# Performance work log

Hardware: AMD Instinct MI355X
Metric: run time of the kernel (lower is better)

## Reference

```python
import jax, jax.numpy as jnp
import numpy as np

B, T, F, E = 256, 256, 8, 128
H = 2 * E  # hidden_dim = 2*embedding_dim = 256
NL = 5     # num_layers per LSTM stack


def setup_inputs() -> dict:
    key = jax.random.key(0)
    ks = jax.random.split(key, 9)
    s1 = 1.0 / np.sqrt(H)
    s2 = 1.0 / np.sqrt(E)
    u = lambda k, shape, s: jax.random.uniform(k, shape, jnp.float32, -s, s)
    return {
        "x": jax.random.normal(ks[0], (B, T, F), jnp.float32),
        # stack 1: input F -> hidden H, 5 layers. b = b_ih + b_hh combined.
        "w_ih0_1": u(ks[1], (4 * H, F), s1),
        "w_ihr_1": u(ks[2], (NL - 1, 4 * H, H), s1),
        "w_hh_1": u(ks[3], (NL, 4 * H, H), s1),
        "b_1": u(ks[4], (NL, 4 * H), s1),
        # stack 2: input H -> hidden E, 5 layers
        "w_ih0_2": u(ks[5], (4 * E, H), s2),
        "w_ihr_2": u(ks[6], (NL - 1, 4 * E, E), s2),
        "w_hh_2": u(ks[7], (NL, 4 * E, E), s2),
        "b_2": u(ks[8], (NL, 4 * E), s2),
    }


def _lstm_layer(x, w_ih, w_hh, b):
    """x: [B,T,D] -> (outputs [B,T,Hd], final hidden [B,Hd]). PyTorch gate order i,f,g,o."""
    Hd = w_hh.shape[-1]
    # precompute input contribution for all timesteps (the big GEMM)
    xg = jnp.einsum('btd,gd->tbg', x, w_ih) + b  # [T,B,4Hd]
    h0 = jnp.zeros((x.shape[0], Hd), x.dtype)

    def step(carry, xt):
        h, c = carry
        g = xt + h @ w_hh.T
        i, f, gg, o = jnp.split(g, 4, axis=-1)
        c = jax.nn.sigmoid(f) * c + jax.nn.sigmoid(i) * jnp.tanh(gg)
        h = jax.nn.sigmoid(o) * jnp.tanh(c)
        return (h, c), h

    (h, _), hs = jax.lax.scan(step, (h0, h0), xg)
    return jnp.swapaxes(hs, 0, 1), h


def _stack(x, w_ih0, w_ihr, w_hh, b):
    y, h = _lstm_layer(x, w_ih0, w_hh[0], b[0])
    for l in range(1, w_hh.shape[0]):
        y, h = _lstm_layer(y, w_ihr[l - 1], w_hh[l], b[l])
    return y, h


def reference(x, w_ih0_1, w_ihr_1, w_hh_1, b_1, w_ih0_2, w_ihr_2, w_hh_2, b_2):
    x = x.reshape(x.shape[0], T, F)
    y, _ = _stack(x, w_ih0_1, w_ihr_1, w_hh_1, b_1)   # [B,T,H]
    _, h = _stack(y, w_ih0_2, w_ihr_2, w_hh_2, b_2)   # h: [B,E] last layer final hidden
    return h
```

## Files before the change

kernel.cpp:

```cpp
#include <hip/hip_runtime.h>
#include <math.h>

typedef unsigned short u16;
typedef unsigned int   u32;
typedef unsigned long long u64;
typedef __bf16 bf16x8 __attribute__((ext_vector_type(8)));
typedef float  f32x4  __attribute__((ext_vector_type(4)));

#define BB 256
#define TT 256
#define HD 256
#define ED 128
#define DEPTH 8
#define NE 73

#define HRING   (10 * DEPTH * BB * HD / 2)
#define CTR_OFF (2 * HRING)
#define GRP_OFF (CTR_OFF + 512)
#define XP_U32  (BB * TT * 8 / 2)
#define XPH_OFF (GRP_OFF + 640)
#define XPL_OFF (XPH_OFF + XP_U32)
#define WT_OFF  (XPL_OFF + XP_U32)

__constant__ size_t g_woff[10] = {0ul,589824ul,1638400ul,2686976ul,3735552ul,
                                  4784128ul,5177344ul,5439488ul,5701632ul,5963776ul};
__constant__ int g_cb[11] = {0,73728,204800,335872,466944,598016,
                             647168,679936,712704,745472,778240};

__device__ __forceinline__ u16 f2bf_hi(float f) {
    u32 u = __float_as_uint(f);
    u32 r = (u + 0x7FFFu + ((u >> 16) & 1u)) >> 16;
    return (u16)r;
}
__device__ __forceinline__ float bf2f(u16 h) { return __uint_as_float(((u32)h) << 16); }
__device__ __forceinline__ float sigmoidf_(float v) { return 1.0f / (1.0f + expf(-v)); }

__global__ __launch_bounds__(256) void zero_state(u32* wsd) {
    const int n = XPH_OFF;
    for (int i = blockIdx.x * blockDim.x + threadIdx.x; i < n; i += gridDim.x * blockDim.x)
        wsd[i] = 0u;
}

__global__ __launch_bounds__(256) void conv_x(const float* __restrict__ x, u32* __restrict__ wsd) {
    u16* xph = (u16*)(wsd + XPH_OFF);
    u16* xpl = (u16*)(wsd + XPL_OFF);
    const int n = BB * TT * 8;
    for (int i = blockIdx.x * blockDim.x + threadIdx.x; i < n; i += gridDim.x * blockDim.x) {
        float v = x[i];
        u16 hi = f2bf_hi(v);
        xph[i] = hi;
        xpl[i] = f2bf_hi(v - bf2f(hi));
    }
}

__global__ __launch_bounds__(256) void conv_all(
    const float* __restrict__ w_ih0_1, const float* __restrict__ w_ihr_1,
    const float* __restrict__ w_hh_1,
    const float* __restrict__ w_ih0_2, const float* __restrict__ w_ihr_2,
    const float* __restrict__ w_hh_2,
    u32* __restrict__ wsd)
{
    __bf16* dst0 = (__bf16*)(wsd + WT_OFF);
    const int nch = 778240;
    for (int ci = blockIdx.x * blockDim.x + threadIdx.x; ci < nch;
         ci += gridDim.x * blockDim.x) {
        int l = 0;
        while (ci >= g_cb[l + 1]) ++l;
        int di = ci - g_cb[l];

        const int hd  = (l < 5) ? 256 : 128;
        const int din = (l == 0) ? 32 : ((l < 6) ? 256 : 128);
        const int xw  = (l == 0) ? 8 : din;
        const int Kp  = din + hd;
        const int nk  = Kp >> 5;

        const float *wih, *whh; int wihld, whhld;
        if (l == 0)      { wih = w_ih0_1;                                whh = w_hh_1;
                           wihld = 8;   whhld = 256; }
        else if (l < 5)  { wih = w_ihr_1 + (size_t)(l - 1) * 1024 * 256; whh = w_hh_1 + (size_t)l * 1024 * 256;
                           wihld = 256; whhld = 256; }
        else if (l == 5) { wih = w_ih0_2;                                whh = w_hh_2;
                           wihld = 256; whhld = 128; }
        else             { wih = w_ihr_2 + (size_t)(l - 6) * 512 * 128;  whh = w_hh_2 + (size_t)(l - 5) * 512 * 128;
                           wihld = 128; whhld = 128; }

        int lane = di & 63;
        int rem  = di >> 6;
        int kt   = rem % nk;
        int rem2 = rem / nk;
        int p    = rem2 & 1;
        int g    = (rem2 >> 1) & 3;
        int jt   = rem2 >> 3;
        int r15  = lane & 15, kq = lane >> 4;
        int row  = g * hd + jt * 16 + r15;

        bf16x8 o8;
        #pragma unroll
        for (int e = 0; e < 8; ++e) {
            int k = kt * 32 + kq * 8 + e;
            float v = 0.0f;
            if (k < xw) v = wih[(size_t)row * wihld + k];
            else if (k >= din && k < Kp) v = whh[(size_t)row * whhld + (k - din)];
            __bf16 h = (__bf16)v;
            o8[e] = p ? (__bf16)(v - (float)h) : h;
        }
        *(bf16x8*)(dst0 + g_woff[l] + (size_t)di * 8) = o8;
    }
}

template<int NKI, int NKT, bool ISL0>
__device__ void run_persist(int l, int bid, int xcd, int jt, int bt, int hd, u32 arr7,
    int ng, u32* __restrict__ gflg,
    const float* __restrict__ bias, u32* __restrict__ wsd, u32* __restrict__ ctr,
    float* __restrict__ out, const u16* __restrict__ A_sh)
{
    constexpr int DIN = NKI * 32;
    constexpr int RS  = (NKT < 4) ? NKT : 4;

    u16* hhi = (u16*)wsd;
    u16* hlo = (u16*)(wsd + HRING);
    const u16* xph = (const u16*)(wsd + XPH_OFF);
    const u16* xpl = (const u16*)(wsd + XPL_OFF);

    const int tid  = threadIdx.x;
    const int lane = tid & 63;
    const int wv   = tid >> 6;
    const int r15  = lane & 15;
    const int kqc  = lane >> 4;
    const int brow = bt * 128 + wv * 16 + r15;
    const int j0   = jt * 16 + kqc * 4;

    float bgr[4][4];
    #pragma unroll
    for (int g = 0; g < 4; ++g) {
        float4 v = *(const float4*)&bias[g * hd + j0];
        bgr[g][0] = v.x; bgr[g][1] = v.y; bgr[g][2] = v.z; bgr[g][3] = v.w;
    }

    int offH[4], offL[4];
    #pragma unroll
    for (int g = 0; g < 4; ++g) {
        offH[g] = (g * 2)     * NKT * 512 + lane * 8;
        offL[g] = (g * 2 + 1) * NKT * 512 + lane * 8;
    }

    float4 cv = make_float4(0.f, 0.f, 0.f, 0.f);
    const int lm = (l > 0) ? (l - 1) : 0;

    auto STEP = [&](int t) {
        const size_t sIn   = ((size_t)lm * DEPTH + (t & 7)) * (BB * HD);
        const size_t sPrev = ((size_t)l * DEPTH + ((t - 1) & 7)) * (BB * HD);
        const size_t sOut  = ((size_t)l * DEPTH + (t & 7)) * (BB * HD);

        auto ldB = [&](int kt, uint4& H4, uint4& L4) {
            if constexpr (ISL0) {
                if (kt == 0) {
                    if (kqc == 0) {
                        const size_t xo = ((size_t)brow * TT + t) * 8;
                        H4 = *(const uint4*)(xph + xo);
                        L4 = *(const uint4*)(xpl + xo);
                    } else { H4 = make_uint4(0,0,0,0); L4 = make_uint4(0,0,0,0); }
                } else {
                    const size_t o = sPrev + (size_t)brow * HD + (kt * 32 - 32) + kqc * 8;
                    H4 = *(const uint4*)(hhi + o);
                    L4 = *(const uint4*)(hlo + o);
                }
            } else {
                const int k0 = kt * 32 + kqc * 8;
                const size_t o = (k0 < DIN) ? (sIn + (size_t)brow * HD + k0)
                                            : (sPrev + (size_t)brow * HD + (k0 - DIN));
                H4 = *(const uint4*)(hhi + o);
                L4 = *(const uint4*)(hlo + o);
            }
        };

        f32x4 acc0 = {0.f,0.f,0.f,0.f}, acc1 = {0.f,0.f,0.f,0.f};
        f32x4 acc2 = {0.f,0.f,0.f,0.f}, acc3 = {0.f,0.f,0.f,0.f};

        uint4 ra[RS], rb[RS];
        #pragma unroll
        for (int i = 0; i < RS; ++i) ldB(i, ra[i], rb[i]);

        #pragma unroll
        for (int kt = 0; kt < NKT; ++kt) {
            union { uint4 u; bf16x8 v; } BH, BL;
            BH.u = ra[kt % RS]; BL.u = rb[kt % RS];
            bf16x8 bh = BH.v, bl = BL.v;
            if (kt + RS < NKT) ldB(kt + RS, ra[kt % RS], rb[kt % RS]);

            const int kof = kt * 512;
            bf16x8 a0h = *(const bf16x8*)&A_sh[offH[0] + kof];
            bf16x8 a1h = *(const bf16x8*)&A_sh[offH[1] + kof];
            bf16x8 a2h = *(const bf16x8*)&A_sh[offH[2] + kof];
            bf16x8 a3h = *(const bf16x8*)&A_sh[offH[3] + kof];
            bf16x8 a0l = *(const bf16x8*)&A_sh[offL[0] + kof];
            bf16x8 a1l = *(const bf16x8*)&A_sh[offL[1] + kof];
            bf16x8 a2l = *(const bf16x8*)&A_sh[offL[2] + kof];
            bf16x8 a3l = *(const bf16x8*)&A_sh[offL[3] + kof];

            acc0 = __builtin_amdgcn_mfma_f32_16x16x32_bf16(a0h, bh, acc0, 0, 0, 0);
            acc1 = __builtin_amdgcn_mfma_f32_16x16x32_bf16(a1h, bh, acc1, 0, 0, 0);
            acc2 = __builtin_amdgcn_mfma_f32_16x16x32_bf16(a2h, bh, acc2, 0, 0, 0);
            acc3 = __builtin_amdgcn_mfma_f32_16x16x32_bf16(a3h, bh, acc3, 0, 0, 0);
            acc0 = __builtin_amdgcn_mfma_f32_16x16x32_bf16(a0h, bl, acc0, 0, 0, 0);
            acc1 = __builtin_amdgcn_mfma_f32_16x16x32_bf16(a1h, bl, acc1, 0, 0, 0);
            acc2 = __builtin_amdgcn_mfma_f32_16x16x32_bf16(a2h, bl, acc2, 0, 0, 0);
            acc3 = __builtin_amdgcn_mfma_f32_16x16x32_bf16(a3h, bl, acc3, 0, 0, 0);
            acc0 = __builtin_amdgcn_mfma_f32_16x16x32_bf16(a0l, bh, acc0, 0, 0, 0);
            acc1 = __builtin_amdgcn_mfma_f32_16x16x32_bf16(a1l, bh, acc1, 0, 0, 0);
            acc2 = __builtin_amdgcn_mfma_f32_16x16x32_bf16(a2l, bh, acc2, 0, 0, 0);
            acc3 = __builtin_amdgcn_mfma_f32_16x16x32_bf16(a3l, bh, acc3, 0, 0, 0);
        }

        float4 hv;
        {
            float i_, f_, g_, o_;
            i_ = sigmoidf_(acc0[0] + bgr[0][0]); f_ = sigmoidf_(acc1[0] + bgr[1][0]);
            g_ = tanhf   (acc2[0] + bgr[2][0]); o_ = sigmoidf_(acc3[0] + bgr[3][0]);
            cv.x = fmaf(f_, cv.x, i_ * g_); hv.x = o_ * tanhf(cv.x);
            i_ = sigmoidf_(acc0[1] + bgr[0][1]); f_ = sigmoidf_(acc1[1] + bgr[1][1]);
            g_ = tanhf   (acc2[1] + bgr[2][1]); o_ = sigmoidf_(acc3[1] + bgr[3][1]);
            cv.y = fmaf(f_, cv.y, i_ * g_); hv.y = o_ * tanhf(cv.y);
            i_ = sigmoidf_(acc0[2] + bgr[0][2]); f_ = sigmoidf_(acc1[2] + bgr[1][2]);
            g_ = tanhf   (acc2[2] + bgr[2][2]); o_ = sigmoidf_(acc3[2] + bgr[3][2]);
            cv.z = fmaf(f_, cv.z, i_ * g_); hv.z = o_ * tanhf(cv.z);
            i_ = sigmoidf_(acc0[3] + bgr[0][3]); f_ = sigmoidf_(acc1[3] + bgr[1][3]);
            g_ = tanhf   (acc2[3] + bgr[2][3]); o_ = sigmoidf_(acc3[3] + bgr[3][3]);
            cv.w = fmaf(f_, cv.w, i_ * g_); hv.w = o_ * tanhf(cv.w);
        }

        u16 h0 = f2bf_hi(hv.x), h1 = f2bf_hi(hv.y), h2 = f2bf_hi(hv.z), h3 = f2bf_hi(hv.w);
        u64 hiP = (u64)h0 | ((u64)h1 << 16) | ((u64)h2 << 32) | ((u64)h3 << 48);
        u64 loP = (u64)f2bf_hi(hv.x - bf2f(h0)) |
                  ((u64)f2bf_hi(hv.y - bf2f(h1)) << 16) |
                  ((u64)f2bf_hi(hv.z - bf2f(h2)) << 32) |
                  ((u64)f2bf_hi(hv.w - bf2f(h3)) << 48);
        const size_t ho = sOut + (size_t)brow * HD + j0;
        __hip_atomic_store((u64*)(hhi + ho), hiP, __ATOMIC_RELAXED, __HIP_MEMORY_SCOPE_AGENT);
        __hip_atomic_store((u64*)(hlo + ho), loP, __ATOMIC_RELAXED, __HIP_MEMORY_SCOPE_AGENT);

        if (l == 9 && t == TT - 1)
            *(float4*)&out[(size_t)brow * ED + j0] = hv;
    };

    for (int E = 0; E < NE; ++E) {
        const int ep = E - l;
        if (ep >= 0 && ep < 64) {
            #pragma unroll 1
            for (int i = 0; i < 4; ++i) {
                const int t = 4 * ep + i;
                if (i > 0) {
                    if (tid == 0) {
                        const u32 tg = (u32)ng * (u32)(3 * ep + i);
                        for (int it = 0; it < (1 << 20); ++it) {
                            if (__hip_atomic_load(gflg, __ATOMIC_RELAXED,
                                                  __HIP_MEMORY_SCOPE_AGENT) >= tg) break;
                            __builtin_amdgcn_s_sleep(1);
                        }
                    }
                    __syncthreads();
                }
                STEP(t);
                if (i < 3) {
                    __syncthreads();
                    if (tid == 0)
                        __hip_atomic_fetch_add(gflg, 1u, __ATOMIC_RELAXED, __HIP_MEMORY_SCOPE_AGENT);
                }
            }
        }

        __syncthreads();
        if (tid == 0) {
            __hip_atomic_fetch_add(&ctr[xcd * 32], 1u,
                                   __ATOMIC_RELAXED, __HIP_MEMORY_SCOPE_AGENT);
            const u32 w1 = (u32)(E + 1);
            if (bid == 0) {
                for (int it = 0; it < (1 << 22); ++it) {
                    bool ok = true;
                    #pragma unroll
                    for (int r = 0; r < 8; ++r) {
                        u32 tgt = ((r == 7) ? arr7 : 32u) * w1;
                        ok &= (__hip_atomic_load(&ctr[r * 32], __ATOMIC_RELAXED,
                                                 __HIP_MEMORY_SCOPE_AGENT) >= tgt);
                    }
                    if (ok) break;
                    __builtin_amdgcn_s_sleep(1);
                }
                __hip_atomic_store(&ctr[256], w1, __ATOMIC_RELAXED, __HIP_MEMORY_SCOPE_AGENT);
            } else {
                for (int it = 0; it < (1 << 22); ++it) {
                    if (__hip_atomic_load(&ctr[256], __ATOMIC_RELAXED,
                                          __HIP_MEMORY_SCOPE_AGENT) >= w1) break;
                    __builtin_amdgcn_s_sleep(1);
                }
            }
            __builtin_amdgcn_fence(__ATOMIC_ACQUIRE, "agent");
        }
        __syncthreads();
    }
}

__global__ __launch_bounds__(512, 2) void lstm_persist(
    const float* __restrict__ b_1, const float* __restrict__ b_2,
    u32* __restrict__ wsd, float* __restrict__ out)
{
    __shared__ __align__(16) u16 A_sh[65536];

    const int bid = blockIdx.x;
    const int xcd = bid & 7, slot = bid >> 3;
    int l, jt, bt;
    if (xcd < 5)      { l = xcd;               bt = slot >> 4;        jt = slot & 15; }
    else if (xcd == 5){ l = 5 + (slot >> 4);   bt = (slot >> 3) & 1;  jt = slot & 7; }
    else if (xcd == 6){ l = 7 + (slot >> 4);   bt = (slot >> 3) & 1;  jt = slot & 7; }
    else              { if (slot >= 16) return; l = 9; bt = slot >> 3; jt = slot & 7; }

    const int hd  = (l < 5) ? 256 : 128;
    const int din = (l == 0) ? 32 : ((l < 6) ? 256 : 128);
    const int nk  = (din + hd) >> 5;
    const float* bias = (l < 5) ? (b_1 + l * 1024) : (b_2 + (l - 5) * 512);

    u32* ctr  = wsd + CTR_OFF;
    u32* gflg = wsd + GRP_OFF + (size_t)(l * 2 + bt) * 32;
    const u16* wt = (const u16*)(wsd + WT_OFF);

    const int ng = (l < 5) ? 16 : 8;

    {
        const uint4* src = (const uint4*)(wt + g_woff[l] + (size_t)jt * 8 * nk * 512);
        uint4* dst = (uint4*)A_sh;
        const int n4 = nk * 512;
        for (int i = threadIdx.x; i < n4; i += 512) dst[i] = src[i];
    }
    __syncthreads();

    if (l == 0)
        run_persist<1, 9, true >(l, bid, xcd, jt, bt, hd, 16u, ng, gflg, bias, wsd, ctr, out, A_sh);
    else if (l < 5)
        run_persist<8, 16, false>(l, bid, xcd, jt, bt, hd, 16u, ng, gflg, bias, wsd, ctr, out, A_sh);
    else if (l == 5)
        run_persist<8, 12, false>(l, bid, xcd, jt, bt, hd, 16u, ng, gflg, bias, wsd, ctr, out, A_sh);
    else
        run_persist<4, 8, false>(l, bid, xcd, jt, bt, hd, 16u, ng, gflg, bias, wsd, ctr, out, A_sh);
}

extern "C" void kernel_launch(void* const* d_in, const int* in_sizes, int n_in,
                              void* d_out, int out_size, void* d_ws, size_t ws_size,
                              hipStream_t stream) {
    const float* x       = (const float*)d_in[0];
    const float* w_ih0_1 = (const float*)d_in[1];
    const float* w_ihr_1 = (const float*)d_in[2];
    const float* w_hh_1  = (const float*)d_in[3];
    const float* b_1     = (const float*)d_in[4];
    const float* w_ih0_2 = (const float*)d_in[5];
    const float* w_ihr_2 = (const float*)d_in[6];
    const float* w_hh_2  = (const float*)d_in[7];
    const float* b_2     = (const float*)d_in[8];
    u32*   wsd = (u32*)d_ws;
    float* out = (float*)d_out;

    hipLaunchKernelGGL(zero_state, dim3(1024), dim3(256), 0, stream, wsd);
    hipLaunchKernelGGL(conv_all, dim3(1024), dim3(256), 0, stream,
                       w_ih0_1, w_ihr_1, w_hh_1, w_ih0_2, w_ihr_2, w_hh_2, wsd);
    hipLaunchKernelGGL(conv_x, dim3(256), dim3(256), 0, stream, x, wsd);
    hipLaunchKernelGGL(lstm_persist, dim3(256), dim3(512), 0, stream,
                       b_1, b_2, wsd, out);
}
```

Before: 2.890 ms.

## Hoist input-projection MFMAs off the recurrent critical path, pairing two timesteps

Splits each LSTM step into an input-projection part and a recurrent part. The input contribution for two consecutive timesteps is computed together before the inter-block wait, so each weight fragment loaded from LDS feeds two B operands. Only the recurrent h·W_hh part stays between the grid-flag waits, which shortens the serialized per-step chain. The cost is a second set of accumulators, which raises register pressure and may lower occupancy or cause spills.

```diff
diff --git a/kernel.cpp b/kernel.cpp
--- a/kernel.cpp
+++ b/kernel.cpp
@@ -34,6 +34,9 @@
 }
 __device__ __forceinline__ float bf2f(u16 h) { return __uint_as_float(((u32)h) << 16); }
 __device__ __forceinline__ float sigmoidf_(float v) { return 1.0f / (1.0f + expf(-v)); }
+__device__ __forceinline__ bf16x8 asbf8(const uint4& u) {
+    union { uint4 u; bf16x8 v; } c; c.u = u; return c.v;
+}
 
 __global__ __launch_bounds__(256) void zero_state(u32* wsd) {
     const int n = XPH_OFF;
@@ -114,8 +117,9 @@
     const float* __restrict__ bias, u32* __restrict__ wsd, u32* __restrict__ ctr,
     float* __restrict__ out, const u16* __restrict__ A_sh)
 {
-    constexpr int DIN = NKI * 32;
-    constexpr int RS  = (NKT < 4) ? NKT : 4;
+    constexpr int NKR = NKT - NKI;
+    constexpr int RS  = (NKR < 4) ? NKR : 4;
+    constexpr int RSI = (NKI < 3) ? NKI : 3;
 
     u16* hhi = (u16*)wsd;
     u16* hlo = (u16*)(wsd + HRING);
@@ -147,85 +151,136 @@
     float4 cv = make_float4(0.f, 0.f, 0.f, 0.f);
     const int lm = (l > 0) ? (l - 1) : 0;
 
-    auto STEP = [&](int t) {
-        const size_t sIn   = ((size_t)lm * DEPTH + (t & 7)) * (BB * HD);
+    auto MF12 = [&](int kof, const bf16x8& bh, const bf16x8& bl, f32x4 (&ac)[4]) {
+        bf16x8 a0h = *(const bf16x8*)&A_sh[offH[0] + kof];
+        bf16x8 a1h = *(const bf16x8*)&A_sh[offH[1] + kof];
+        bf16x8 a2h = *(const bf16x8*)&A_sh[offH[2] + kof];
+        bf16x8 a3h = *(const bf16x8*)&A_sh[offH[3] + kof];
+        bf16x8 a0l = *(const bf16x8*)&A_sh[offL[0] + kof];
+        bf16x8 a1l = *(const bf16x8*)&A_sh[offL[1] + kof];
+        bf16x8 a2l = *(const bf16x8*)&A_sh[offL[2] + kof];
+        bf16x8 a3l = *(const bf16x8*)&A_sh[offL[3] + kof];
+        ac[0] = __builtin_amdgcn_mfma_f32_16x16x32_bf16(a0h, bh, ac[0], 0, 0, 0);
+        ac[1] = __builtin_amdgcn_mfma_f32_16x16x32_bf16(a1h, bh, ac[1], 0, 0, 0);
+        ac[2] = __builtin_amdgcn_mfma_f32_16x16x32_bf16(a2h, bh, ac[2], 0, 0, 0);
+        ac[3] = __builtin_amdgcn_mfma_f32_16x16x32_bf16(a3h, bh, ac[3], 0, 0, 0);
+        ac[0] = __builtin_amdgcn_mfma_f32_16x16x32_bf16(a0h, bl, ac[0], 0, 0, 0);
+        ac[1] = __builtin_amdgcn_mfma_f32_16x16x32_bf16(a1h, bl, ac[1], 0, 0, 0);
+        ac[2] = __builtin_amdgcn_mfma_f32_16x16x32_bf16(a2h, bl, ac[2], 0, 0, 0);
+        ac[3] = __builtin_amdgcn_mfma_f32_16x16x32_bf16(a3h, bl, ac[3], 0, 0, 0);
+        ac[0] = __builtin_amdgcn_mfma_f32_16x16x32_bf16(a0l, bh, ac[0], 0, 0, 0);
+        ac[1] = __builtin_amdgcn_mfma_f32_16x16x32_bf16(a1l, bh, ac[1], 0, 0, 0);
+        ac[2] = __builtin_amdgcn_mfma_f32_16x16x32_bf16(a2l, bh, ac[2], 0, 0, 0);
+        ac[3] = __builtin_amdgcn_mfma_f32_16x16x32_bf16(a3l, bh, ac[3], 0, 0, 0);
+    };
+    auto MF24 = [&](int kof, const bf16x8& b0h, const bf16x8& b0l,
+                    const bf16x8& b1h, const bf16x8& b1l,
+                    f32x4 (&a0)[4], f32x4 (&a1)[4]) {
+        bf16x8 a0h = *(const bf16x8*)&A_sh[offH[0] + kof];
+        bf16x8 a1hh = *(const bf16x8*)&A_sh[offH[1] + kof];
+        bf16x8 a2h = *(const bf16x8*)&A_sh[offH[2] + kof];
+        bf16x8 a3h = *(const bf16x8*)&A_sh[offH[3] + kof];
+        bf16x8 a0l = *(const bf16x8*)&A_sh[offL[0] + kof];
+        bf16x8 a1l = *(const bf16x8*)&A_sh[offL[1] + kof];
+        bf16x8 a2l = *(const bf16x8*)&A_sh[offL[2] + kof];
+        bf16x8 a3l = *(const bf16x8*)&A_sh[offL[3] + kof];
+        a0[0] = __builtin_amdgcn_mfma_f32_16x16x32_bf16(a0h,  b0h, a0[0], 0, 0, 0);
+        a1[0] = __builtin_amdgcn_mfma_f32_16x16x32_bf16(a0h,  b1h, a1[0], 0, 0, 0);
+        a0[1] = __builtin_amdgcn_mfma_f32_16x16x32_bf16(a1hh, b0h, a0[1], 0, 0, 0);
+        a1[1] = __builtin_amdgcn_mfma_f32_16x16x32_bf16(a1hh, b1h, a1[1], 0, 0, 0);
+        a0[2] = __builtin_amdgcn_mfma_f32_16x16x32_bf16(a2h,  b0h, a0[2], 0, 0, 0);
+        a1[2] = __builtin_amdgcn_mfma_f32_16x16x32_bf16(a2h,  b1h, a1[2], 0, 0, 0);
+        a0[3] = __builtin_amdgcn_mfma_f32_16x16x32_bf16(a3h,  b0h, a0[3], 0, 0, 0);
+        a1[3] = __builtin_amdgcn_mfma_f32_16x16x32_bf16(a3h,  b1h, a1[3], 0, 0, 0);
+        a0[0] = __builtin_amdgcn_mfma_f32_16x16x32_bf16(a0h,  b0l, a0[0], 0, 0, 0);
+        a1[0] = __builtin_amdgcn_mfma_f32_16x16x32_bf16(a0h,  b1l, a1[0], 0, 0, 0);
+        a0[1] = __builtin_amdgcn_mfma_f32_16x16x32_bf16(a1hh, b0l, a0[1], 0, 0, 0);
+        a1[1] = __builtin_amdgcn_mfma_f32_16x16x32_bf16(a1hh, b1l, a1[1], 0, 0, 0);
+        a0[2] = __builtin_amdgcn_mfma_f32_16x16x32_bf16(a2h,  b0l, a0[2], 0, 0, 0);
+        a1[2] = __builtin_amdgcn_mfma_f32_16x16x32_bf16(a2h,  b1l, a1[2], 0, 0, 0);
+        a0[3] = __builtin_amdgcn_mfma_f32_16x16x32_bf16(a3h,  b0l, a0[3], 0, 0, 0);
+        a1[3] = __builtin_amdgcn_mfma_f32_16x16x32_bf16(a3h,  b1l, a1[3], 0, 0, 0);
+        a0[0] = __builtin_amdgcn_mfma_f32_16x16x32_bf16(a0l,  b0h, a0[0], 0, 0, 0);
+        a1[0] = __builtin_amdgcn_mfma_f32_16x16x32_bf16(a0l,  b1h, a1[0], 0, 0, 0);
+        a0[1] = __builtin_amdgcn_mfma_f32_16x16x32_bf16(a1l,  b0h, a0[1], 0, 0, 0);
+        a1[1] = __builtin_amdgcn_mfma_f32_16x16x32_bf16(a1l,  b1h, a1[1], 0, 0, 0);
+        a0[2] = __builtin_amdgcn_mfma_f32_16x16x32_bf16(a2l,  b0h, a0[2], 0, 0, 0);
+        a1[2] = __builtin_amdgcn_mfma_f32_16x16x32_bf16(a2l,  b1h, a1[2], 0, 0, 0);
+        a0[3] = __builtin_amdgcn_mfma_f32_16x16x32_bf16(a3l,  b0h, a0[3], 0, 0, 0);
+        a1[3] = __builtin_amdgcn_mfma_f32_16x16x32_bf16(a3l,  b1h, a1[3], 0, 0, 0);
+    };
+
+    auto DUAL_IN = [&](int t0, f32x4 (&a0)[4], f32x4 (&a1)[4]) {
+        if constexpr (ISL0) {
+            uint4 h0, l0q, h1, l1q;
+            if (kqc == 0) {
+                const size_t x0 = ((size_t)brow * TT + t0) * 8;
+                const size_t x1 = ((size_t)brow * TT + t0 + 1) * 8;
+                h0 = *(const uint4*)(xph + x0); l0q = *(const uint4*)(xpl + x0);
+                h1 = *(const uint4*)(xph + x1); l1q = *(const uint4*)(xpl + x1);
+            } else {
+                h0 = make_uint4(0,0,0,0); l0q = h0; h1 = h0; l1q = h0;
+            }
+            MF24(0, asbf8(h0), asbf8(l0q), asbf8(h1), asbf8(l1q), a0, a1);
+        } else {
+            const size_t sIn0 = ((size_t)lm * DEPTH + (t0 & 7)) * (BB * HD);
+            const size_t sIn1 = ((size_t)lm * DEPTH + ((t0 + 1) & 7)) * (BB * HD);
+            auto ldBI = [&](size_t sIn, int kt, uint4& H4, uint4& L4) {
+                const size_t o = sIn + (size_t)brow * HD + kt * 32 + kqc * 8;
+                H4 = *(const uint4*)(hhi + o);
+                L4 = *(const uint4*)(hlo + o);
+            };
+            uint4 p0a[RSI], p0b[RSI], p1a[RSI], p1b[RSI];
+            #pragma unroll
+            for (int i = 0; i < RSI; ++i) {
+                ldBI(sIn0, i, p0a[i], p0b[i]);
+                ldBI(sIn1, i, p1a[i], p1b[i]);
+            }
+            #pragma unroll
+            for (int kt = 0; kt < NKI; ++kt) {
+                bf16x8 b0h = asbf8(p0a[kt % RSI]), b0l = asbf8(p0b[kt % RSI]);
+                bf16x8 b1h = asbf8(p1a[kt % RSI]), b1l = asbf8(p1b[kt % RSI]);
+                if (kt + RSI < NKI) {
+                    ldBI(sIn0, kt + RSI, p0a[kt % RSI], p0b[kt % RSI]);
+                    ldBI(sIn1, kt + RSI, p1a[kt % RSI], p1b[kt % RSI]);
+                }
+                MF24(kt * 512, b0h, b0l, b1h, b1l, a0, a1);
+            }
+        }
+    };
+
+    auto REC_STEP = [&](int t, f32x4 (&ac)[4]) {
         const size_t sPrev = ((size_t)l * DEPTH + ((t - 1) & 7)) * (BB * HD);
         const size_t sOut  = ((size_t)l * DEPTH + (t & 7)) * (BB * HD);
-
-        auto ldB = [&](int kt, uint4& H4, uint4& L4) {
-            if constexpr (ISL0) {
-                if (kt == 0) {
-                    if (kqc == 0) {
-                        const size_t xo = ((size_t)brow * TT + t) * 8;
-                        H4 = *(const uint4*)(xph + xo);
-                        L4 = *(const uint4*)(xpl + xo);
-                    } else { H4 = make_uint4(0,0,0,0); L4 = make_uint4(0,0,0,0); }
-                } else {
-                    const size_t o = sPrev + (size_t)brow * HD + (kt * 32 - 32) + kqc * 8;
-                    H4 = *(const uint4*)(hhi + o);
-                    L4 = *(const uint4*)(hlo + o);
-                }
-            } else {
-                const int k0 = kt * 32 + kqc * 8;
-                const size_t o = (k0 < DIN) ? (sIn + (size_t)brow * HD + k0)
-                                            : (sPrev + (size_t)brow * HD + (k0 - DIN));
-                H4 = *(const uint4*)(hhi + o);
-                L4 = *(const uint4*)(hlo + o);
-            }
+        auto ldBR = [&](int kt, uint4& H4, uint4& L4) {
+            const size_t o = sPrev + (size_t)brow * HD + (kt - NKI) * 32 + kqc * 8;
+            H4 = *(const uint4*)(hhi + o);
+            L4 = *(const uint4*)(hlo + o);
         };
-
-        f32x4 acc0 = {0.f,0.f,0.f,0.f}, acc1 = {0.f,0.f,0.f,0.f};
-        f32x4 acc2 = {0.f,0.f,0.f,0.f}, acc3 = {0.f,0.f,0.f,0.f};
-
         uint4 ra[RS], rb[RS];
         #pragma unroll
-        for (int i = 0; i < RS; ++i) ldB(i, ra[i], rb[i]);
-
+        for (int i = 0; i < RS; ++i) ldBR(NKI + i, ra[i], rb[i]);
         #pragma unroll
-        for (int kt = 0; kt < NKT; ++kt) {
-            union { uint4 u; bf16x8 v; } BH, BL;
-            BH.u = ra[kt % RS]; BL.u = rb[kt % RS];
-            bf16x8 bh = BH.v, bl = BL.v;
-            if (kt + RS < NKT) ldB(kt + RS, ra[kt % RS], rb[kt % RS]);
-
-            const int kof = kt * 512;
-            bf16x8 a0h = *(const bf16x8*)&A_sh[offH[0] + kof];
-            bf16x8 a1h = *(const bf16x8*)&A_sh[offH[1] + kof];
-            bf16x8 a2h = *(const bf16x8*)&A_sh[offH[2] + kof];
-            bf16x8 a3h = *(const bf16x8*)&A_sh[offH[3] + kof];
-            bf16x8 a0l = *(const bf16x8*)&A_sh[offL[0] + kof];
-            bf16x8 a1l = *(const bf16x8*)&A_sh[offL[1] + kof];
-            bf16x8 a2l = *(const bf16x8*)&A_sh[offL[2] + kof];
-            bf16x8 a3l = *(const bf16x8*)&A_sh[offL[3] + kof];
-
-            acc0 = __builtin_amdgcn_mfma_f32_16x16x32_bf16(a0h, bh, acc0, 0, 0, 0);
-            acc1 = __builtin_amdgcn_mfma_f32_16x16x32_bf16(a1h, bh, acc1, 0, 0, 0);
-            acc2 = __builtin_amdgcn_mfma_f32_16x16x32_bf16(a2h, bh, acc2, 0, 0, 0);
-            acc3 = __builtin_amdgcn_mfma_f32_16x16x32_bf16(a3h, bh, acc3, 0, 0, 0);
-            acc0 = __builtin_amdgcn_mfma_f32_16x16x32_bf16(a0h, bl, acc0, 0, 0, 0);
-            acc1 = __builtin_amdgcn_mfma_f32_16x16x32_bf16(a1h, bl, acc1, 0, 0, 0);
-            acc2 = __builtin_amdgcn_mfma_f32_16x16x32_bf16(a2h, bl, acc2, 0, 0, 0);
-            acc3 = __builtin_amdgcn_mfma_f32_16x16x32_bf16(a3h, bl, acc3, 0, 0, 0);
-            acc0 = __builtin_amdgcn_mfma_f32_16x16x32_bf16(a0l, bh, acc0, 0, 0, 0);
-            acc1 = __builtin_amdgcn_mfma_f32_16x16x32_bf16(a1l, bh, acc1, 0, 0, 0);
-            acc2 = __builtin_amdgcn_mfma_f32_16x16x32_bf16(a2l, bh, acc2, 0, 0, 0);
-            acc3 = __builtin_amdgcn_mfma_f32_16x16x32_bf16(a3l, bh, acc3, 0, 0, 0);
+        for (int kt = NKI; kt < NKT; ++kt) {
+            bf16x8 bh = asbf8(ra[(kt - NKI) % RS]), bl = asbf8(rb[(kt - NKI) % RS]);
+            if (kt + RS < NKT) ldBR(kt + RS, ra[(kt - NKI) % RS], rb[(kt - NKI) % RS]);
+            MF12(kt * 512, bh, bl, ac);
         }
 
         float4 hv;
         {
             float i_, f_, g_, o_;
-            i_ = sigmoidf_(acc0[0] + bgr[0][0]); f_ = sigmoidf_(acc1[0] + bgr[1][0]);
-            g_ = tanhf   (acc2[0] + bgr[2][0]); o_ = sigmoidf_(acc3[0] + bgr[3][0]);
+            i_ = sigmoidf_(ac[0][0] + bgr[0][0]); f_ = sigmoidf_(ac[1][0] + bgr[1][0]);
+            g_ = tanhf   (ac[2][0] + bgr[2][0]); o_ = sigmoidf_(ac[3][0] + bgr[3][0]);
             cv.x = fmaf(f_, cv.x, i_ * g_); hv.x = o_ * tanhf(cv.x);
-            i_ = sigmoidf_(acc0[1] + bgr[0][1]); f_ = sigmoidf_(acc1[1] + bgr[1][1]);
-            g_ = tanhf   (acc2[1] + bgr[2][1]); o_ = sigmoidf_(acc3[1] + bgr[3][1]);
+            i_ = sigmoidf_(ac[0][1] + bgr[0][1]); f_ = sigmoidf_(ac[1][1] + bgr[1][1]);
+            g_ = tanhf   (ac[2][1] + bgr[2][1]); o_ = sigmoidf_(ac[3][1] + bgr[3][1]);
             cv.y = fmaf(f_, cv.y, i_ * g_); hv.y = o_ * tanhf(cv.y);
-            i_ = sigmoidf_(acc0[2] + bgr[0][2]); f_ = sigmoidf_(acc1[2] + bgr[1][2]);
-            g_ = tanhf   (acc2[2] + bgr[2][2]); o_ = sigmoidf_(acc3[2] + bgr[3][2]);
+            i_ = sigmoidf_(ac[0][2] + bgr[0][2]); f_ = sigmoidf_(ac[1][2] + bgr[1][2]);
+            g_ = tanhf   (ac[2][2] + bgr[2][2]); o_ = sigmoidf_(ac[3][2] + bgr[3][2]);
             cv.z = fmaf(f_, cv.z, i_ * g_); hv.z = o_ * tanhf(cv.z);
-            i_ = sigmoidf_(acc0[3] + bgr[0][3]); f_ = sigmoidf_(acc1[3] + bgr[1][3]);
-            g_ = tanhf   (acc2[3] + bgr[2][3]); o_ = sigmoidf_(acc3[3] + bgr[3][3]);
+            i_ = sigmoidf_(ac[0][3] + bgr[0][3]); f_ = sigmoidf_(ac[1][3] + bgr[1][3]);
+            g_ = tanhf   (ac[2][3] + bgr[2][3]); o_ = sigmoidf_(ac[3][3] + bgr[3][3]);
             cv.w = fmaf(f_, cv.w, i_ * g_); hv.w = o_ * tanhf(cv.w);
         }
 
@@ -243,29 +298,46 @@
             *(float4*)&out[(size_t)brow * ED + j0] = hv;
     };
 
+    auto gpost = [&]() {
+        __syncthreads();
+        if (tid == 0)
+            __hip_atomic_fetch_add(gflg, 1u, __ATOMIC_RELAXED, __HIP_MEMORY_SCOPE_AGENT);
+    };
+    auto gwait = [&](u32 tg) {
+        if (tid == 0) {
+            for (int it = 0; it < (1 << 20); ++it) {
+                if (__hip_atomic_load(gflg, __ATOMIC_RELAXED,
+                                      __HIP_MEMORY_SCOPE_AGENT) >= tg) break;
+                __builtin_amdgcn_s_sleep(1);
+            }
+        }
+        __syncthreads();
+    };
+
     for (int E = 0; E < NE; ++E) {
         const int ep = E - l;
         if (ep >= 0 && ep < 64) {
-            #pragma unroll 1
-            for (int i = 0; i < 4; ++i) {
-                const int t = 4 * ep + i;
-                if (i > 0) {
-                    if (tid == 0) {
-                        const u32 tg = (u32)ng * (u32)(3 * ep + i);
-                        for (int it = 0; it < (1 << 20); ++it) {
-                            if (__hip_atomic_load(gflg, __ATOMIC_RELAXED,
-                                                  __HIP_MEMORY_SCOPE_AGENT) >= tg) break;
-                            __builtin_amdgcn_s_sleep(1);
-                        }
-                    }
-                    __syncthreads();
-                }
-                STEP(t);
-                if (i < 3) {
-                    __syncthreads();
-                    if (tid == 0)
-                        __hip_atomic_fetch_add(gflg, 1u, __ATOMIC_RELAXED, __HIP_MEMORY_SCOPE_AGENT);
-                }
+            {
+                f32x4 ia0[4], ia1[4];
+                #pragma unroll
+                for (int g = 0; g < 4; ++g) { ia0[g] = (f32x4){0.f,0.f,0.f,0.f}; ia1[g] = (f32x4){0.f,0.f,0.f,0.f}; }
+                DUAL_IN(4 * ep, ia0, ia1);
+                REC_STEP(4 * ep, ia0);
+                gpost();
+                gwait((u32)ng * (u32)(3 * ep + 1));
+                REC_STEP(4 * ep + 1, ia1);
+                gpost();
+            }
+            {
+                f32x4 ia0[4], ia1[4];
+                #pragma unroll
+                for (int g = 0; g < 4; ++g) { ia0[g] = (f32x4){0.f,0.f,0.f,0.f}; ia1[g] = (f32x4){0.f,0.f,0.f,0.f}; }
+                DUAL_IN(4 * ep + 2, ia0, ia1);
+                gwait((u32)ng * (u32)(3 * ep + 2));
+                REC_STEP(4 * ep + 2, ia0);
+                gpost();
+                gwait((u32)ng * (u32)(3 * ep + 3));
+                REC_STEP(4 * ep + 3, ia1);
             }
         }
 
```

Result: no change. 2.886 ms (-0.1%).
